# Optimization experiments

Hardware: AMD Instinct MI355X
Metric: run time of the kernel (lower is better)

Reference implementation:

```python
import jax, jax.numpy as jnp
import numpy as np

N = 50000   # nodes
E = 600000  # edges (before self-loops)
D = 128     # input_dim
H = 128     # hidden_dim
NEG_SLOPE = 0.2  # GATConv default


def setup_inputs() -> dict:
    key = jax.random.key(0)
    ks = jax.random.split(key, 16)
    inp = {
        "x": jax.random.normal(ks[0], (N, D), jnp.float32),
        "edge_index": jax.random.randint(ks[1], (2, E), 0, N, dtype=jnp.int64),
        "edge_attr": jax.random.normal(ks[2], (E, 1), jnp.float32),
    }
    # GATConv params per layer: lin W [H,in] (no bias), att_src/att_dst [H],
    # lin_edge We [H,1] (no bias), att_edge [H], final bias b [H]
    def mk(k, shape, fan_in):
        return jax.random.normal(k, shape, jnp.float32) / np.sqrt(fan_in)
    ins = [D, H]
    ki = 3
    for i in range(2):
        cin = ins[i]
        inp[f"W{i}"] = mk(ks[ki], (H, cin), cin); ki += 1
        inp[f"att_src{i}"] = mk(ks[ki], (H,), H); ki += 1
        inp[f"att_dst{i}"] = mk(ks[ki], (H,), H); ki += 1
        inp[f"We{i}"] = mk(ks[ki], (H, 1), 1); ki += 1
        inp[f"att_e{i}"] = mk(ks[ki], (H,), H); ki += 1
        inp[f"b{i}"] = jnp.zeros((H,), jnp.float32)
    return inp


def _gat_forward(x, edge_index, edge_attr, params):
    # add self loops; self-loop edge_attr = mean of edge_attr (fill_value='mean')
    src = jnp.concatenate([edge_index[0], jnp.arange(N, dtype=edge_index.dtype)])
    dst = jnp.concatenate([edge_index[1], jnp.arange(N, dtype=edge_index.dtype)])
    ea = jnp.concatenate(
        [edge_attr, jnp.broadcast_to(edge_attr.mean(0, keepdims=True), (N, 1))], 0
    )  # [E+N, 1]

    def gat_layer(h, W, b, a_s, a_d, We, a_e):
        hp = h @ W.T                                   # [N, H]
        e_lin = ea @ We.T                              # [E+N, H]
        alpha = (hp @ a_s)[src] + (hp @ a_d)[dst] + e_lin @ a_e  # [E+N]
        alpha = jax.nn.leaky_relu(alpha, NEG_SLOPE)
        # segment softmax over destination nodes
        m = jax.ops.segment_max(alpha, dst, num_segments=N)
        m = jnp.where(jnp.isfinite(m), m, 0.0)
        w = jnp.exp(alpha - m[dst])
        denom = jax.ops.segment_sum(w, dst, num_segments=N)
        w = w / (denom[dst] + 1e-16)
        out = jax.ops.segment_sum(hp[src] * w[:, None], dst, num_segments=N)
        return out + b

    layer_outs = [x]
    h = x
    for i in range(2):
        h = jax.nn.relu(
            gat_layer(h, params[f"W{i}"], params[f"b{i}"], params[f"att_src{i}"],
                      params[f"att_dst{i}"], params[f"We{i}"], params[f"att_e{i}"])
        )
        layer_outs.append(h)
    return jnp.concatenate(layer_outs, axis=-1)  # JK 'cat': [N, D + 2H]


def reference(x, edge_index, edge_attr,
              W0, att_src0, att_dst0, We0, att_e0, b0,
              W1, att_src1, att_dst1, We1, att_e1, b1):
    params = {
        "W0": W0, "att_src0": att_src0, "att_dst0": att_dst0, "We0": We0,
        "att_e0": att_e0, "b0": b0,
        "W1": W1, "att_src1": att_src1, "att_dst1": att_dst1, "We1": We1,
        "att_e1": att_e1, "b1": b1,
    }
    return _gat_forward(x, edge_index, edge_attr, params)
```

## Files before the change

### kernel.cpp

```cpp
#include <hip/hip_runtime.h>
#include <hip/hip_fp16.h>
#include <math.h>

#define N_NODES 50000
#define N_EDGES 600000
#define TOT (N_EDGES + N_NODES)
#define HD 128
#define OUTW 384
#define NEG_SLOPE 0.2f


typedef _Float16 h2_t __attribute__((ext_vector_type(2)));

static __device__ __forceinline__ float fdot2f(h2_t a, h2_t b, float c){
#if __has_builtin(__builtin_amdgcn_fdot2)
  return __builtin_amdgcn_fdot2(a, b, c, false);
#else
  return fmaf((float)a[0], (float)b[0], fmaf((float)a[1], (float)b[1], c));
#endif
}

static __device__ __forceinline__ int load_edge(const void* ei, int is64, long long off){
  return is64 ? (int)((const long long*)ei)[off] : ((const int*)ei)[off];
}


__global__ __launch_bounds__(256) void prep_kernel(const void* ei, int* flag,
                                                   const float* __restrict__ We0, const float* __restrict__ ae0,
                                                   const float* __restrict__ We1, const float* __restrict__ ae1,
                                                   float* scal, const float* __restrict__ eattr){
  int t = threadIdx.x;
  if (blockIdx.x == 0){
    __shared__ float buf[128];
    __shared__ int okbuf;
    if (t == 0) okbuf = 1;
    __syncthreads();
    if (t < 64){
      long long v = ((const long long*)ei)[t];
      if (v < 0 || v >= N_NODES) atomicAnd(&okbuf, 0);
    }
    if (t < 128) buf[t] = We0[t] * ae0[t];
    __syncthreads();
    for (int off = 64; off > 0; off >>= 1){ if (t < off) buf[t] += buf[t + off]; __syncthreads(); }
    if (t == 0) scal[1] = buf[0];
    __syncthreads();
    if (t < 128) buf[t] = We1[t] * ae1[t];
    __syncthreads();
    for (int off = 64; off > 0; off >>= 1){ if (t < off) buf[t] += buf[t + off]; __syncthreads(); }
    if (t == 0){ scal[2] = buf[0]; *flag = okbuf; }
  }
  int tid = blockIdx.x * 256 + t;
  float s = 0.f;
  for (int i = tid; i < N_EDGES; i += 256 * 256) s += eattr[i];
  for (int off = 32; off > 0; off >>= 1) s += __shfl_down(s, off, 64);
  __shared__ float ws[4];
  int lane = t & 63, w = t >> 6;
  if (lane == 0) ws[w] = s;
  __syncthreads();
  if (t == 0) atomicAdd(&scal[0], ws[0] + ws[1] + ws[2] + ws[3]);
}

#define XBLK 6250
#define WBLK 64
#define DBLK 2540
__global__ __launch_bounds__(256) void conv_kernel(const float* __restrict__ x,
                                                   __half* __restrict__ x16,
                                                   float* __restrict__ out,
                                                   const float* __restrict__ W0, const float* __restrict__ W1,
                                                   __half2* __restrict__ Wt0, __half2* __restrict__ Wt1,
                                                   const void* ei, const int* flag, int* deg,
                                                   int* __restrict__ src32, int* __restrict__ dst32){
  int b = blockIdx.x;
  if (b < XBLK){
    int idx = b * 256 + threadIdx.x;
    int n = idx >> 5, c4 = idx & 31;
    float4 v = ((const float4*)x)[idx];
    *(float4*)&out[(size_t)n * OUTW + c4 * 4] = v;
    float2 pk;
    ((__half2*)&pk)[0] = __floats2half2_rn(v.x, v.y);
    ((__half2*)&pk)[1] = __floats2half2_rn(v.z, v.w);
    *(float2*)&x16[(size_t)idx * 4] = pk;
  } else if (b < XBLK + WBLK){
    int e = (b - XBLK) * 256 + threadIdx.x;
    const float* W = (e < 8192) ? W0 : W1;
    __half2* Wt = (e < 8192) ? Wt0 : Wt1;
    int i = e & 8191;
    int n = i & 127, k2 = i >> 7;
    float a = W[n * HD + 2 * k2];
    float c = W[n * HD + 2 * k2 + 1];
    Wt[k2 * 128 + n] = __floats2half2_rn(a, c);
  } else {
    int e = (b - XBLK - WBLK) * 256 + threadIdx.x;
    if (e >= TOT) return;
    int is64 = *flag;
    int d;
    if (e < N_EDGES){
      int s = load_edge(ei, is64, e);
      d = load_edge(ei, is64, (long long)N_EDGES + e);
      src32[e] = s;
      dst32[e] = d;
    } else {
      d = e - N_EDGES;
    }
    atomicAdd(&deg[d], 1);
  }
}

__global__ __launch_bounds__(256) void scan_chunk_kernel(const int* __restrict__ deg,
                                                         int* __restrict__ rowstart,
                                                         int* __restrict__ chunksums){
  __shared__ int sums[256];
  int t = threadIdx.x;
  int base = blockIdx.x * 1024 + t * 4;
  int v[4];
  #pragma unroll
  for (int i = 0; i < 4; i++) v[i] = (base + i < N_NODES) ? deg[base + i] : 0;
  int tsum = v[0] + v[1] + v[2] + v[3];
  sums[t] = tsum;
  __syncthreads();
  for (int off = 1; off < 256; off <<= 1){
    int add = (t >= off) ? sums[t - off] : 0;
    __syncthreads();
    sums[t] += add;
    __syncthreads();
  }
  int run = sums[t] - tsum;
  #pragma unroll
  for (int i = 0; i < 4; i++){
    if (base + i < N_NODES) rowstart[base + i] = run;
    run += v[i];
  }
  if (t == 255) chunksums[blockIdx.x] = sums[255];
}

__global__ __launch_bounds__(256) void add_off_kernel(int* rowstart, int* rowcur,
                                                      const int* __restrict__ chunksums){
  __shared__ int soff;
  int t = threadIdx.x;
  if (t < 64){
    int v = (t < blockIdx.x) ? chunksums[t] : 0;
    for (int o = 32; o > 0; o >>= 1) v += __shfl_down(v, o, 64);
    if (t == 0) soff = v;
  }
  __syncthreads();
  int off = soff;
  int base = blockIdx.x * 1024 + t * 4;
  #pragma unroll
  for (int i = 0; i < 4; i++){
    if (base + i < N_NODES){
      int v = rowstart[base + i] + off;
      rowstart[base + i] = v;
      rowcur[base + i] = v;
    }
  }
}

__global__ __launch_bounds__(256) void fill_kernel(const int* __restrict__ src32,
                                                   const int* __restrict__ dst32,
                                                   int* rowcur, int2* __restrict__ csr){
  int e = blockIdx.x * 256 + threadIdx.x;
  if (e >= TOT) return;
  int s, d;
  if (e < N_EDGES){
    s = src32[e];
    d = dst32[e];
  } else {
    s = d = e - N_EDGES;
  }
  int pos = atomicAdd(&rowcur[d], 1);
  csr[pos] = make_int2(s, e);
}


#define BM 128

__global__ __launch_bounds__(256, 2) void gemm_kernel(const __half* __restrict__ hin,
                                                      const __half2* __restrict__ Wt,
                                                      __half* __restrict__ hp_h,
                                                      const float* __restrict__ as_,
                                                      const float* __restrict__ ad_,
                                                      float* __restrict__ ssrc,
                                                      float* __restrict__ sdst){
  __shared__ __half2 As2[64 * 128];
  __shared__ __half2 Wh2[64 * 128];
  int t  = threadIdx.x;
  int tx = t & 15;
  int ty = t >> 4;
  int rb = blockIdx.x * BM;

  {
    const float4* src = (const float4*)Wt;
    float4* dst = (float4*)Wh2;
    #pragma unroll
    for (int p = 0; p < 8; p++) dst[t + p * 256] = src[t + p * 256];
  }
  #pragma unroll
  for (int p = 0; p < 8; p++){
    int idx = t + p * 256;
    int row = idx >> 4, c8 = idx & 15;
    int gr = rb + row; if (gr >= N_NODES) gr = N_NODES - 1;
    float4 v = *(const float4*)&hin[(size_t)gr * HD + c8 * 8];
    __half2* hv = (__half2*)&v;
    #pragma unroll
    for (int q = 0; q < 4; q++) As2[(4 * c8 + q) * 128 + row] = hv[q];
  }
  __syncthreads();

  float acc[8][8];
  #pragma unroll
  for (int i = 0; i < 8; i++)
    #pragma unroll
    for (int j = 0; j < 8; j++) acc[i][j] = 0.f;

  #pragma unroll 4
  for (int k2 = 0; k2 < 64; k2++){
    float4 ar0 = *(const float4*)&As2[k2 * 128 + ty * 8];
    float4 ar1 = *(const float4*)&As2[k2 * 128 + ty * 8 + 4];
    float4 wr0 = *(const float4*)&Wh2[k2 * 128 + tx * 4];
    float4 wr1 = *(const float4*)&Wh2[k2 * 128 + 64 + tx * 4];
    const h2_t* av0 = (const h2_t*)&ar0;
    const h2_t* av1 = (const h2_t*)&ar1;
    const h2_t* wv0 = (const h2_t*)&wr0;
    const h2_t* wv1 = (const h2_t*)&wr1;
    #pragma unroll
    for (int i = 0; i < 8; i++){
      h2_t ai = (i < 4) ? av0[i] : av1[i - 4];
      #pragma unroll
      for (int j = 0; j < 4; j++){
        acc[i][j]     = fdot2f(ai, wv0[j], acc[i][j]);
        acc[i][j + 4] = fdot2f(ai, wv1[j], acc[i][j + 4]);
      }
    }
  }

  #pragma unroll
  for (int i = 0; i < 8; i++){
    int r = rb + ty * 8 + i;
    if (r < N_NODES){
      float2 s0, s1;
      ((__half2*)&s0)[0] = __floats2half2_rn(acc[i][0], acc[i][1]);
      ((__half2*)&s0)[1] = __floats2half2_rn(acc[i][2], acc[i][3]);
      ((__half2*)&s1)[0] = __floats2half2_rn(acc[i][4], acc[i][5]);
      ((__half2*)&s1)[1] = __floats2half2_rn(acc[i][6], acc[i][7]);
      *(float2*)&hp_h[(size_t)r * HD + tx * 4]      = s0;
      *(float2*)&hp_h[(size_t)r * HD + 64 + tx * 4] = s1;
    }
  }

  float as_v[8], ad_v[8];
  #pragma unroll
  for (int j = 0; j < 4; j++){
    as_v[j]     = as_[tx * 4 + j];      ad_v[j]     = ad_[tx * 4 + j];
    as_v[j + 4] = as_[64 + tx * 4 + j]; ad_v[j + 4] = ad_[64 + tx * 4 + j];
  }
  #pragma unroll
  for (int i = 0; i < 8; i++){
    float ps = 0.f, pd = 0.f;
    #pragma unroll
    for (int j = 0; j < 8; j++){
      ps = fmaf(acc[i][j], as_v[j], ps);
      pd = fmaf(acc[i][j], ad_v[j], pd);
    }
    #pragma unroll
    for (int off = 8; off > 0; off >>= 1){
      ps += __shfl_down(ps, off, 16);
      pd += __shfl_down(pd, off, 16);
    }
    int r = rb + ty * 8 + i;
    if (tx == 0 && r < N_NODES){ ssrc[r] = ps; sdst[r] = pd; }
  }
}

__global__ __launch_bounds__(256) void agg_kernel(const int* __restrict__ rowstart,
                                                  const int2* __restrict__ csr,
                                                  const float* __restrict__ eattr,
                                                  const float* __restrict__ ssrc,
                                                  const float* __restrict__ sdst,
                                                  const float* __restrict__ scal, int which,
                                                  const __half* __restrict__ hp_h,
                                                  const float* __restrict__ bias,
                                                  __half* __restrict__ hnext,
                                                  float* __restrict__ out, int outoff){
  int sub  = threadIdx.x >> 4;
  int lane = threadIdx.x & 15;
  int n = blockIdx.x * 16 + sub;
  if (n >= N_NODES) return;
  int s0 = rowstart[n];
  int s1 = (n + 1 < N_NODES) ? rowstart[n + 1] : TOT;
  float sd = sdst[n];
  float ce = scal[1 + which];
  float mean_ea = scal[0] * (1.0f / (float)N_EDGES);
  const float4* hb = (const float4*)hp_h;

  float a0 = 0.f, a1 = 0.f, a2 = 0.f, a3 = 0.f;
  float a4 = 0.f, a5 = 0.f, a6 = 0.f, a7 = 0.f;
  float sum = 0.f;

#define EW(se) ({ float eav = ((se).y < N_EDGES) ? eattr[(se).y] : mean_ea;       \
    float al = ssrc[(se).x] + sd + eav * ce;                                      \
    al = (al >= 0.f) ? al : NEG_SLOPE * al;                                       \
    expf(al); })

#define ACC8(r, p) { const __half2* hh = (const __half2*)&(r); float2 f;         \
    f = __half22float2(hh[0]); a0 = fmaf(p, f.x, a0); a1 = fmaf(p, f.y, a1);     \
    f = __half22float2(hh[1]); a2 = fmaf(p, f.x, a2); a3 = fmaf(p, f.y, a3);     \
    f = __half22float2(hh[2]); a4 = fmaf(p, f.x, a4); a5 = fmaf(p, f.y, a5);     \
    f = __half22float2(hh[3]); a6 = fmaf(p, f.x, a6); a7 = fmaf(p, f.y, a7); }

  int i = s0;
  for (; i + 4 <= s1; i += 4){
    int2 se0 = csr[i],     se1 = csr[i + 1];
    int2 se2 = csr[i + 2], se3 = csr[i + 3];
    float4 r0 = hb[(size_t)se0.x * 16 + lane];
    float4 r1 = hb[(size_t)se1.x * 16 + lane];
    float4 r2 = hb[(size_t)se2.x * 16 + lane];
    float4 r3 = hb[(size_t)se3.x * 16 + lane];
    float p0 = EW(se0), p1 = EW(se1), p2 = EW(se2), p3 = EW(se3);
    sum += p0 + p1 + p2 + p3;
    ACC8(r0, p0); ACC8(r1, p1); ACC8(r2, p2); ACC8(r3, p3);
  }
  for (; i < s1; i++){
    int2 se = csr[i];
    float4 r = hb[(size_t)se.x * 16 + lane];
    float p = EW(se);
    sum += p;
    ACC8(r, p);
  }
#undef ACC8
#undef EW

  float inv = 1.0f / (sum + 1e-16f);
  float4 bA = *(const float4*)&bias[lane * 8];
  float4 bB = *(const float4*)&bias[lane * 8 + 4];
  float v0 = fmaf(a0, inv, bA.x); v0 = v0 > 0.f ? v0 : 0.f;
  float v1 = fmaf(a1, inv, bA.y); v1 = v1 > 0.f ? v1 : 0.f;
  float v2 = fmaf(a2, inv, bA.z); v2 = v2 > 0.f ? v2 : 0.f;
  float v3 = fmaf(a3, inv, bA.w); v3 = v3 > 0.f ? v3 : 0.f;
  float v4 = fmaf(a4, inv, bB.x); v4 = v4 > 0.f ? v4 : 0.f;
  float v5 = fmaf(a5, inv, bB.y); v5 = v5 > 0.f ? v5 : 0.f;
  float v6 = fmaf(a6, inv, bB.z); v6 = v6 > 0.f ? v6 : 0.f;
  float v7 = fmaf(a7, inv, bB.w); v7 = v7 > 0.f ? v7 : 0.f;
  if (hnext){
    float4 pk;
    __half2* p2h = (__half2*)&pk;
    p2h[0] = __floats2half2_rn(v0, v1);
    p2h[1] = __floats2half2_rn(v2, v3);
    p2h[2] = __floats2half2_rn(v4, v5);
    p2h[3] = __floats2half2_rn(v6, v7);
    *(float4*)&hnext[(size_t)n * HD + lane * 8] = pk;
  }
  *(float4*)&out[(size_t)n * OUTW + outoff + lane * 8]     = make_float4(v0, v1, v2, v3);
  *(float4*)&out[(size_t)n * OUTW + outoff + lane * 8 + 4] = make_float4(v4, v5, v6, v7);
}


extern "C" void kernel_launch(void* const* d_in, const int* in_sizes, int n_in,
                              void* d_out, int out_size, void* d_ws, size_t ws_size,
                              hipStream_t stream){
  (void)in_sizes; (void)n_in; (void)out_size; (void)ws_size;
  const float* x    = (const float*)d_in[0];
  const void*  ei   = d_in[1];
  const float* eatt = (const float*)d_in[2];
  const float* W0   = (const float*)d_in[3];
  const float* as0  = (const float*)d_in[4];
  const float* ad0  = (const float*)d_in[5];
  const float* We0  = (const float*)d_in[6];
  const float* ae0  = (const float*)d_in[7];
  const float* b0   = (const float*)d_in[8];
  const float* W1   = (const float*)d_in[9];
  const float* as1  = (const float*)d_in[10];
  const float* ad1  = (const float*)d_in[11];
  const float* We1  = (const float*)d_in[12];
  const float* ae1  = (const float*)d_in[13];
  const float* b1   = (const float*)d_in[14];
  float* out = (float*)d_out;

  char* ws = (char*)d_ws;
  size_t off = 0;
  auto alloc = [&](size_t bytes) -> void* {
    void* p = ws + off;
    off += (bytes + 255) & ~(size_t)255;
    return p;
  };
  __half*   hp_h     = (__half*)  alloc((size_t)N_NODES * HD * 2);
  __half*   h1       = (__half*)  alloc((size_t)N_NODES * HD * 2);
  __half*   x16      = (__half*)  alloc((size_t)N_NODES * HD * 2);
  float*    ssrc     = (float*)   alloc((size_t)N_NODES * 4);
  float*    sdst     = (float*)   alloc((size_t)N_NODES * 4);
  int*      deg      = (int*)     alloc((size_t)N_NODES * 4);
  float*    scal     = (float*)   alloc(64 * 4);
  int*      rowstart = (int*)     alloc((size_t)N_NODES * 4);
  int*      rowcur   = (int*)     alloc((size_t)N_NODES * 4);
  int*      src32    = (int*)     alloc((size_t)N_EDGES * 4);
  int*      dst32    = (int*)     alloc((size_t)N_EDGES * 4);
  int2*     csr      = (int2*)    alloc((size_t)TOT * 8);
  __half2*  Wt0      = (__half2*) alloc((size_t)8192 * 4);
  __half2*  Wt1      = (__half2*) alloc((size_t)8192 * 4);
  int*      chunksums= (int*)     alloc(64 * 4);
  int*      flag     = (int*)     alloc(64);

  hipMemsetAsync(deg, 0, 200192 + 256, stream);

  const int nchunks = (N_NODES + 1023) / 1024;
  const int FB = (TOT + 255) / 256;

  prep_kernel<<<256, 256, 0, stream>>>(ei, flag, We0, ae0, We1, ae1, scal, eatt);
  conv_kernel<<<XBLK + WBLK + DBLK, 256, 0, stream>>>(x, x16, out, W0, W1, Wt0, Wt1,
                                                      ei, flag, deg, src32, dst32);
  scan_chunk_kernel<<<nchunks, 256, 0, stream>>>(deg, rowstart, chunksums);
  add_off_kernel<<<nchunks, 256, 0, stream>>>(rowstart, rowcur, chunksums);
  fill_kernel<<<FB, 256, 0, stream>>>(src32, dst32, rowcur, csr);

  const int GB = (N_NODES + BM - 1) / BM;
  const int NB16 = (N_NODES + 15) / 16;

  gemm_kernel<<<GB, 256, 0, stream>>>(x16, Wt0, hp_h, as0, ad0, ssrc, sdst);
  agg_kernel<<<NB16, 256, 0, stream>>>(rowstart, csr, eatt, ssrc, sdst, scal, 0, hp_h, b0, h1, out, 128);

  gemm_kernel<<<GB, 256, 0, stream>>>(h1, Wt1, hp_h, as1, ad1, ssrc, sdst);
  agg_kernel<<<NB16, 256, 0, stream>>>(rowstart, csr, eatt, ssrc, sdst, scal, 1, hp_h, b1, nullptr, out, 256);
}
```

Before: 324.6 us.

## Fuse all GAT stages into one persistent kernel with grid-wide barriers

Replaces the nine separate launches (prep, convert, scan, offset, fill, two GEMMs, two aggregations) with a single persistent kernel of 512 blocks. Stages are separated by a software grid barrier built on atomic counters. The aim is to remove per-launch overhead and idle gaps between small kernels. The aggregation inner loop is also unrolled to 8 edges to give more gathers in flight. In exchange, each stage is capped at 512 resident blocks, and the barrier assumes all blocks are co-resident; it has a spin timeout that could silently break ordering.

```diff
diff --git a/kernel.cpp b/kernel.cpp
--- a/kernel.cpp
+++ b/kernel.cpp
@@ -9,6 +9,14 @@
 #define OUTW 384
 #define NEG_SLOPE 0.2f
 
+#define GRID 512
+#define NTHR 256
+#define GSZ (GRID * NTHR)
+#define NCHUNK 49
+#define BM 128
+#define GB 391
+#define AGB 3125
+
 
 typedef _Float16 h2_t __attribute__((ext_vector_type(2)));
 
@@ -24,97 +32,111 @@
   return is64 ? (int)((const long long*)ei)[off] : ((const int*)ei)[off];
 }
 
-
-__global__ __launch_bounds__(256) void prep_kernel(const void* ei, int* flag,
-                                                   const float* __restrict__ We0, const float* __restrict__ ae0,
-                                                   const float* __restrict__ We1, const float* __restrict__ ae1,
-                                                   float* scal, const float* __restrict__ eattr){
-  int t = threadIdx.x;
-  if (blockIdx.x == 0){
-    __shared__ float buf[128];
-    __shared__ int okbuf;
-    if (t == 0) okbuf = 1;
-    __syncthreads();
-    if (t < 64){
-      long long v = ((const long long*)ei)[t];
-      if (v < 0 || v >= N_NODES) atomicAnd(&okbuf, 0);
-    }
-    if (t < 128) buf[t] = We0[t] * ae0[t];
-    __syncthreads();
-    for (int off = 64; off > 0; off >>= 1){ if (t < off) buf[t] += buf[t + off]; __syncthreads(); }
-    if (t == 0) scal[1] = buf[0];
-    __syncthreads();
-    if (t < 128) buf[t] = We1[t] * ae1[t];
-    __syncthreads();
-    for (int off = 64; off > 0; off >>= 1){ if (t < off) buf[t] += buf[t + off]; __syncthreads(); }
-    if (t == 0){ scal[2] = buf[0]; *flag = okbuf; }
-  }
-  int tid = blockIdx.x * 256 + t;
-  float s = 0.f;
-  for (int i = tid; i < N_EDGES; i += 256 * 256) s += eattr[i];
-  for (int off = 32; off > 0; off >>= 1) s += __shfl_down(s, off, 64);
-  __shared__ float ws[4];
-  int lane = t & 63, w = t >> 6;
-  if (lane == 0) ws[w] = s;
-  __syncthreads();
-  if (t == 0) atomicAdd(&scal[0], ws[0] + ws[1] + ws[2] + ws[3]);
-}
-
-#define XBLK 6250
-#define WBLK 64
-#define DBLK 2540
-__global__ __launch_bounds__(256) void conv_kernel(const float* __restrict__ x,
-                                                   __half* __restrict__ x16,
-                                                   float* __restrict__ out,
-                                                   const float* __restrict__ W0, const float* __restrict__ W1,
-                                                   __half2* __restrict__ Wt0, __half2* __restrict__ Wt1,
-                                                   const void* ei, const int* flag, int* deg,
-                                                   int* __restrict__ src32, int* __restrict__ dst32){
-  int b = blockIdx.x;
-  if (b < XBLK){
-    int idx = b * 256 + threadIdx.x;
+struct MegaArgs {
+  const float* x; const void* ei; const float* eattr;
+  const float* W0; const float* as0; const float* ad0; const float* b0;
+  const float* W1; const float* as1; const float* ad1; const float* b1;
+  const float* We0; const float* ae0; const float* We1; const float* ae1;
+  __half* x16; __half* hp_h; __half* h1;
+  float* ssrc; float* sdst;
+  int* deg; float* scal;
+  int* rowstart; int* rowcur;
+  int* src32; int* dst32; int2* csr;
+  __half2* Wt0; __half2* Wt1; int* chunksums;
+  int* barcnt; int* bargen;
+  float* out;
+};
+
+__device__ __forceinline__ void gbar(int* cnt, int* gen){
+  __syncthreads();
+  if (threadIdx.x == 0){
+    __threadfence();
+    int g = __hip_atomic_load(gen, __ATOMIC_RELAXED, __HIP_MEMORY_SCOPE_AGENT);
+    int arrived = __hip_atomic_fetch_add(cnt, 1, __ATOMIC_ACQ_REL, __HIP_MEMORY_SCOPE_AGENT);
+    if (arrived == GRID - 1){
+      __hip_atomic_store(cnt, 0, __ATOMIC_RELAXED, __HIP_MEMORY_SCOPE_AGENT);
+      __hip_atomic_fetch_add(gen, 1, __ATOMIC_RELEASE, __HIP_MEMORY_SCOPE_AGENT);
+    } else {
+      long long spins = 0;
+      while (__hip_atomic_load(gen, __ATOMIC_RELAXED, __HIP_MEMORY_SCOPE_AGENT) == g){
+        __builtin_amdgcn_s_sleep(2);
+        if (++spins > (1LL << 22)) break;
+      }
+    }
+    __threadfence();
+  }
+  __syncthreads();
+}
+
+
+__device__ __forceinline__ void dev_phase0(int bid, int t, const MegaArgs& a, int* s_is64){
+  if (t < 64){
+    long long v = ((const long long*)a.ei)[t];
+    unsigned long long bad = __ballot(v < 0 || v >= N_NODES);
+    if (t == 0) *s_is64 = (bad == 0ull) ? 1 : 0;
+  }
+  __syncthreads();
+  int is64 = *s_is64;
+  int gtid = bid * NTHR + t;
+
+  for (int idx = gtid; idx < N_NODES * HD / 4; idx += GSZ){
     int n = idx >> 5, c4 = idx & 31;
-    float4 v = ((const float4*)x)[idx];
-    *(float4*)&out[(size_t)n * OUTW + c4 * 4] = v;
+    float4 v = ((const float4*)a.x)[idx];
+    *(float4*)&a.out[(size_t)n * OUTW + c4 * 4] = v;
     float2 pk;
     ((__half2*)&pk)[0] = __floats2half2_rn(v.x, v.y);
     ((__half2*)&pk)[1] = __floats2half2_rn(v.z, v.w);
-    *(float2*)&x16[(size_t)idx * 4] = pk;
-  } else if (b < XBLK + WBLK){
-    int e = (b - XBLK) * 256 + threadIdx.x;
-    const float* W = (e < 8192) ? W0 : W1;
-    __half2* Wt = (e < 8192) ? Wt0 : Wt1;
+    *(float2*)&a.x16[(size_t)idx * 4] = pk;
+  }
+  for (int e = gtid; e < 16384; e += GSZ){
+    const float* W = (e < 8192) ? a.W0 : a.W1;
+    __half2* Wt = (e < 8192) ? a.Wt0 : a.Wt1;
     int i = e & 8191;
     int n = i & 127, k2 = i >> 7;
-    float a = W[n * HD + 2 * k2];
-    float c = W[n * HD + 2 * k2 + 1];
-    Wt[k2 * 128 + n] = __floats2half2_rn(a, c);
-  } else {
-    int e = (b - XBLK - WBLK) * 256 + threadIdx.x;
-    if (e >= TOT) return;
-    int is64 = *flag;
+    float va = W[n * HD + 2 * k2];
+    float vb = W[n * HD + 2 * k2 + 1];
+    Wt[k2 * 128 + n] = __floats2half2_rn(va, vb);
+  }
+  for (int e = gtid; e < TOT; e += GSZ){
     int d;
     if (e < N_EDGES){
-      int s = load_edge(ei, is64, e);
-      d = load_edge(ei, is64, (long long)N_EDGES + e);
-      src32[e] = s;
-      dst32[e] = d;
+      int s = load_edge(a.ei, is64, e);
+      d = load_edge(a.ei, is64, (long long)N_EDGES + e);
+      a.src32[e] = s;
+      a.dst32[e] = d;
     } else {
       d = e - N_EDGES;
     }
-    atomicAdd(&deg[d], 1);
-  }
-}
-
-__global__ __launch_bounds__(256) void scan_chunk_kernel(const int* __restrict__ deg,
-                                                         int* __restrict__ rowstart,
-                                                         int* __restrict__ chunksums){
-  __shared__ int sums[256];
-  int t = threadIdx.x;
-  int base = blockIdx.x * 1024 + t * 4;
+    atomicAdd(&a.deg[d], 1);
+  }
+  {
+    float s = 0.f;
+    for (int i = gtid; i < N_EDGES; i += GSZ) s += a.eattr[i];
+    #pragma unroll
+    for (int o = 32; o > 0; o >>= 1) s += __shfl_down(s, o, 64);
+    if ((t & 63) == 0) atomicAdd(&a.scal[0], s);
+  }
+  if (bid == 0){
+    int w = t >> 6, lane = t & 63;
+    if (w == 1){
+      float s = a.We0[lane] * a.ae0[lane] + a.We0[lane + 64] * a.ae0[lane + 64];
+      #pragma unroll
+      for (int o = 32; o > 0; o >>= 1) s += __shfl_down(s, o, 64);
+      if (lane == 0) a.scal[1] = s;
+    } else if (w == 2){
+      float s = a.We1[lane] * a.ae1[lane] + a.We1[lane + 64] * a.ae1[lane + 64];
+      #pragma unroll
+      for (int o = 32; o > 0; o >>= 1) s += __shfl_down(s, o, 64);
+      if (lane == 0) a.scal[2] = s;
+    }
+  }
+}
+
+__device__ __forceinline__ void dev_scanC(int bid, int t, int* sums, const MegaArgs& a){
+  int base = bid * 1024 + t * 4;
   int v[4];
   #pragma unroll
-  for (int i = 0; i < 4; i++) v[i] = (base + i < N_NODES) ? deg[base + i] : 0;
+  for (int i = 0; i < 4; i++) v[i] = (base + i < N_NODES) ? a.deg[base + i] : 0;
   int tsum = v[0] + v[1] + v[2] + v[3];
   sums[t] = tsum;
   __syncthreads();
@@ -127,66 +149,55 @@
   int run = sums[t] - tsum;
   #pragma unroll
   for (int i = 0; i < 4; i++){
-    if (base + i < N_NODES) rowstart[base + i] = run;
+    if (base + i < N_NODES) a.rowstart[base + i] = run;
     run += v[i];
   }
-  if (t == 255) chunksums[blockIdx.x] = sums[255];
-}
-
-__global__ __launch_bounds__(256) void add_off_kernel(int* rowstart, int* rowcur,
-                                                      const int* __restrict__ chunksums){
-  __shared__ int soff;
-  int t = threadIdx.x;
-  if (t < 64){
-    int v = (t < blockIdx.x) ? chunksums[t] : 0;
-    for (int o = 32; o > 0; o >>= 1) v += __shfl_down(v, o, 64);
-    if (t == 0) soff = v;
-  }
-  __syncthreads();
-  int off = soff;
-  int base = blockIdx.x * 1024 + t * 4;
+  if (t == 255) a.chunksums[bid] = sums[255];
+}
+
+__device__ __forceinline__ void dev_offD(int bid, int t, const MegaArgs& a){
+  int lane = t & 63;
+  int v = (lane < bid) ? a.chunksums[lane] : 0;
+  #pragma unroll
+  for (int o = 32; o > 0; o >>= 1) v += __shfl_down(v, o, 64);
+  int off = __shfl(v, 0, 64);
+  int base = bid * 1024 + t * 4;
   #pragma unroll
   for (int i = 0; i < 4; i++){
     if (base + i < N_NODES){
-      int v = rowstart[base + i] + off;
-      rowstart[base + i] = v;
-      rowcur[base + i] = v;
-    }
-  }
-}
-
-__global__ __launch_bounds__(256) void fill_kernel(const int* __restrict__ src32,
-                                                   const int* __restrict__ dst32,
-                                                   int* rowcur, int2* __restrict__ csr){
-  int e = blockIdx.x * 256 + threadIdx.x;
-  if (e >= TOT) return;
-  int s, d;
-  if (e < N_EDGES){
-    s = src32[e];
-    d = dst32[e];
-  } else {
-    s = d = e - N_EDGES;
-  }
-  int pos = atomicAdd(&rowcur[d], 1);
-  csr[pos] = make_int2(s, e);
-}
-
-
-#define BM 128
-
-__global__ __launch_bounds__(256, 2) void gemm_kernel(const __half* __restrict__ hin,
-                                                      const __half2* __restrict__ Wt,
-                                                      __half* __restrict__ hp_h,
-                                                      const float* __restrict__ as_,
-                                                      const float* __restrict__ ad_,
-                                                      float* __restrict__ ssrc,
-                                                      float* __restrict__ sdst){
-  __shared__ __half2 As2[64 * 128];
-  __shared__ __half2 Wh2[64 * 128];
-  int t  = threadIdx.x;
+      int r = a.rowstart[base + i] + off;
+      a.rowstart[base + i] = r;
+      a.rowcur[base + i] = r;
+    }
+  }
+}
+
+__device__ __forceinline__ void dev_fillE(int bid, int t, const MegaArgs& a){
+  int gtid = bid * NTHR + t;
+  for (int e = gtid; e < TOT; e += GSZ){
+    int s, d;
+    if (e < N_EDGES){
+      s = a.src32[e];
+      d = a.dst32[e];
+    } else {
+      s = d = e - N_EDGES;
+    }
+    int pos = atomicAdd(&a.rowcur[d], 1);
+    a.csr[pos] = make_int2(s, e);
+  }
+}
+
+__device__ __forceinline__ void dev_gemm_tile(int tb, int t, __half2* As2, __half2* Wh2,
+                                              const __half* __restrict__ hin,
+                                              const __half2* __restrict__ Wt,
+                                              __half* __restrict__ hp_h,
+                                              const float* __restrict__ as_,
+                                              const float* __restrict__ ad_,
+                                              float* __restrict__ ssrc,
+                                              float* __restrict__ sdst){
   int tx = t & 15;
   int ty = t >> 4;
-  int rb = blockIdx.x * BM;
+  int rb = tb * BM;
 
   {
     const float4* src = (const float4*)Wt;
@@ -269,32 +280,37 @@
     int r = rb + ty * 8 + i;
     if (tx == 0 && r < N_NODES){ ssrc[r] = ps; sdst[r] = pd; }
   }
-}
-
-__global__ __launch_bounds__(256) void agg_kernel(const int* __restrict__ rowstart,
-                                                  const int2* __restrict__ csr,
-                                                  const float* __restrict__ eattr,
-                                                  const float* __restrict__ ssrc,
-                                                  const float* __restrict__ sdst,
-                                                  const float* __restrict__ scal, int which,
-                                                  const __half* __restrict__ hp_h,
-                                                  const float* __restrict__ bias,
-                                                  __half* __restrict__ hnext,
-                                                  float* __restrict__ out, int outoff){
-  int sub  = threadIdx.x >> 4;
-  int lane = threadIdx.x & 15;
-  int n = blockIdx.x * 16 + sub;
-  if (n >= N_NODES) return;
-  int s0 = rowstart[n];
-  int s1 = (n + 1 < N_NODES) ? rowstart[n + 1] : TOT;
-  float sd = sdst[n];
+  __syncthreads();
+}
+
+__device__ __forceinline__ void dev_agg(int bid, int t,
+                                        const int* __restrict__ rowstart,
+                                        const int2* __restrict__ csr,
+                                        const float* __restrict__ eattr,
+                                        const float* __restrict__ ssrc,
+                                        const float* __restrict__ sdst,
+                                        const float* __restrict__ scal, int which,
+                                        const __half* __restrict__ hp_h,
+                                        const float* __restrict__ bias,
+                                        __half* __restrict__ hnext,
+                                        float* __restrict__ out, int outoff){
+  int sub  = t >> 4;
+  int lane = t & 15;
   float ce = scal[1 + which];
   float mean_ea = scal[0] * (1.0f / (float)N_EDGES);
+  float4 bA = *(const float4*)&bias[lane * 8];
+  float4 bB = *(const float4*)&bias[lane * 8 + 4];
   const float4* hb = (const float4*)hp_h;
 
-  float a0 = 0.f, a1 = 0.f, a2 = 0.f, a3 = 0.f;
-  float a4 = 0.f, a5 = 0.f, a6 = 0.f, a7 = 0.f;
-  float sum = 0.f;
+  for (int nb = bid; nb < AGB; nb += GRID){
+    int n = nb * 16 + sub;
+    int s0 = rowstart[n];
+    int s1 = (n + 1 < N_NODES) ? rowstart[n + 1] : TOT;
+    float sd = sdst[n];
+
+    float a0 = 0.f, a1 = 0.f, a2 = 0.f, a3 = 0.f;
+    float a4 = 0.f, a5 = 0.f, a6 = 0.f, a7 = 0.f;
+    float sum = 0.f;
 
 #define EW(se) ({ float eav = ((se).y < N_EDGES) ? eattr[(se).y] : mean_ea;       \
     float al = ssrc[(se).x] + sd + eav * ce;                                      \
@@ -307,50 +323,81 @@
     f = __half22float2(hh[2]); a4 = fmaf(p, f.x, a4); a5 = fmaf(p, f.y, a5);     \
     f = __half22float2(hh[3]); a6 = fmaf(p, f.x, a6); a7 = fmaf(p, f.y, a7); }
 
-  int i = s0;
-  for (; i + 4 <= s1; i += 4){
-    int2 se0 = csr[i],     se1 = csr[i + 1];
-    int2 se2 = csr[i + 2], se3 = csr[i + 3];
-    float4 r0 = hb[(size_t)se0.x * 16 + lane];
-    float4 r1 = hb[(size_t)se1.x * 16 + lane];
-    float4 r2 = hb[(size_t)se2.x * 16 + lane];
-    float4 r3 = hb[(size_t)se3.x * 16 + lane];
-    float p0 = EW(se0), p1 = EW(se1), p2 = EW(se2), p3 = EW(se3);
-    sum += p0 + p1 + p2 + p3;
-    ACC8(r0, p0); ACC8(r1, p1); ACC8(r2, p2); ACC8(r3, p3);
-  }
-  for (; i < s1; i++){
-    int2 se = csr[i];
-    float4 r = hb[(size_t)se.x * 16 + lane];
-    float p = EW(se);
-    sum += p;
-    ACC8(r, p);
-  }
+    int i = s0;
+    for (; i + 8 <= s1; i += 8){
+      int2 se[8]; float4 r[8];
+      #pragma unroll
+      for (int u = 0; u < 8; u++) se[u] = csr[i + u];
+      #pragma unroll
+      for (int u = 0; u < 8; u++) r[u] = hb[(size_t)se[u].x * 16 + lane];
+      #pragma unroll
+      for (int u = 0; u < 8; u++){
+        float p = EW(se[u]);
+        sum += p;
+        ACC8(r[u], p);
+      }
+    }
+    for (; i < s1; i++){
+      int2 se = csr[i];
+      float4 r = hb[(size_t)se.x * 16 + lane];
+      float p = EW(se);
+      sum += p;
+      ACC8(r, p);
+    }
 #undef ACC8
 #undef EW
 
-  float inv = 1.0f / (sum + 1e-16f);
-  float4 bA = *(const float4*)&bias[lane * 8];
-  float4 bB = *(const float4*)&bias[lane * 8 + 4];
-  float v0 = fmaf(a0, inv, bA.x); v0 = v0 > 0.f ? v0 : 0.f;
-  float v1 = fmaf(a1, inv, bA.y); v1 = v1 > 0.f ? v1 : 0.f;
-  float v2 = fmaf(a2, inv, bA.z); v2 = v2 > 0.f ? v2 : 0.f;
-  float v3 = fmaf(a3, inv, bA.w); v3 = v3 > 0.f ? v3 : 0.f;
-  float v4 = fmaf(a4, inv, bB.x); v4 = v4 > 0.f ? v4 : 0.f;
-  float v5 = fmaf(a5, inv, bB.y); v5 = v5 > 0.f ? v5 : 0.f;
-  float v6 = fmaf(a6, inv, bB.z); v6 = v6 > 0.f ? v6 : 0.f;
-  float v7 = fmaf(a7, inv, bB.w); v7 = v7 > 0.f ? v7 : 0.f;
-  if (hnext){
-    float4 pk;
-    __half2* p2h = (__half2*)&pk;
-    p2h[0] = __floats2half2_rn(v0, v1);
-    p2h[1] = __floats2half2_rn(v2, v3);
-    p2h[2] = __floats2half2_rn(v4, v5);
-    p2h[3] = __floats2half2_rn(v6, v7);
-    *(float4*)&hnext[(size_t)n * HD + lane * 8] = pk;
-  }
-  *(float4*)&out[(size_t)n * OUTW + outoff + lane * 8]     = make_float4(v0, v1, v2, v3);
-  *(float4*)&out[(size_t)n * OUTW + outoff + lane * 8 + 4] = make_float4(v4, v5, v6, v7);
+    float inv = 1.0f / (sum + 1e-16f);
+    float v0 = fmaf(a0, inv, bA.x); v0 = v0 > 0.f ? v0 : 0.f;
+    float v1 = fmaf(a1, inv, bA.y); v1 = v1 > 0.f ? v1 : 0.f;
+    float v2 = fmaf(a2, inv, bA.z); v2 = v2 > 0.f ? v2 : 0.f;
+    float v3 = fmaf(a3, inv, bA.w); v3 = v3 > 0.f ? v3 : 0.f;
+    float v4 = fmaf(a4, inv, bB.x); v4 = v4 > 0.f ? v4 : 0.f;
+    float v5 = fmaf(a5, inv, bB.y); v5 = v5 > 0.f ? v5 : 0.f;
+    float v6 = fmaf(a6, inv, bB.z); v6 = v6 > 0.f ? v6 : 0.f;
+    float v7 = fmaf(a7, inv, bB.w); v7 = v7 > 0.f ? v7 : 0.f;
+    if (hnext){
+      float4 pk;
+      __half2* p2h = (__half2*)&pk;
+      p2h[0] = __floats2half2_rn(v0, v1);
+      p2h[1] = __floats2half2_rn(v2, v3);
+      p2h[2] = __floats2half2_rn(v4, v5);
+      p2h[3] = __floats2half2_rn(v6, v7);
+      *(float4*)&hnext[(size_t)n * HD + lane * 8] = pk;
+    }
+    *(float4*)&out[(size_t)n * OUTW + outoff + lane * 8]     = make_float4(v0, v1, v2, v3);
+    *(float4*)&out[(size_t)n * OUTW + outoff + lane * 8 + 4] = make_float4(v4, v5, v6, v7);
+  }
+}
+
+
+__global__ __launch_bounds__(256, 2) void mega_kernel(MegaArgs a){
+  __shared__ __align__(16) char smraw[65536];
+  __half2* smA = (__half2*)smraw;
+  __half2* smW = (__half2*)(smraw + 32768);
+  int* isums = (int*)smraw;
+  int* s_is64 = (int*)(smraw + 65280);
+
+  int bid = blockIdx.x, t = threadIdx.x;
+
+  dev_phase0(bid, t, a, s_is64);
+  gbar(a.barcnt, a.bargen);
+  if (bid < NCHUNK) dev_scanC(bid, t, isums, a);
+  gbar(a.barcnt, a.bargen);
+  if (bid < NCHUNK) dev_offD(bid, t, a);
+  gbar(a.barcnt, a.bargen);
+  dev_fillE(bid, t, a);
+  for (int tb = bid; tb < GB; tb += GRID)
+    dev_gemm_tile(tb, t, smA, smW, a.x16, a.Wt0, a.hp_h, a.as0, a.ad0, a.ssrc, a.sdst);
+  gbar(a.barcnt, a.bargen);
+  dev_agg(bid, t, a.rowstart, a.csr, a.eattr, a.ssrc, a.sdst,
+          a.scal, 0, a.hp_h, a.b0, a.h1, a.out, 128);
+  gbar(a.barcnt, a.bargen);
+  for (int tb = bid; tb < GB; tb += GRID)
+    dev_gemm_tile(tb, t, smA, smW, a.h1, a.Wt1, a.hp_h, a.as1, a.ad1, a.ssrc, a.sdst);
+  gbar(a.barcnt, a.bargen);
+  dev_agg(bid, t, a.rowstart, a.csr, a.eattr, a.ssrc, a.sdst,
+          a.scal, 1, a.hp_h, a.b1, nullptr, a.out, 256);
 }
 
 
@@ -358,22 +405,6 @@
                               void* d_out, int out_size, void* d_ws, size_t ws_size,
                               hipStream_t stream){
   (void)in_sizes; (void)n_in; (void)out_size; (void)ws_size;
-  const float* x    = (const float*)d_in[0];
-  const void*  ei   = d_in[1];
-  const float* eatt = (const float*)d_in[2];
-  const float* W0   = (const float*)d_in[3];
-  const float* as0  = (const float*)d_in[4];
-  const float* ad0  = (const float*)d_in[5];
-  const float* We0  = (const float*)d_in[6];
-  const float* ae0  = (const float*)d_in[7];
-  const float* b0   = (const float*)d_in[8];
-  const float* W1   = (const float*)d_in[9];
-  const float* as1  = (const float*)d_in[10];
-  const float* ad1  = (const float*)d_in[11];
-  const float* We1  = (const float*)d_in[12];
-  const float* ae1  = (const float*)d_in[13];
-  const float* b1   = (const float*)d_in[14];
-  float* out = (float*)d_out;
 
   char* ws = (char*)d_ws;
   size_t off = 0;
@@ -382,41 +413,47 @@
     off += (bytes + 255) & ~(size_t)255;
     return p;
   };
-  __half*   hp_h     = (__half*)  alloc((size_t)N_NODES * HD * 2);
-  __half*   h1       = (__half*)  alloc((size_t)N_NODES * HD * 2);
-  __half*   x16      = (__half*)  alloc((size_t)N_NODES * HD * 2);
-  float*    ssrc     = (float*)   alloc((size_t)N_NODES * 4);
-  float*    sdst     = (float*)   alloc((size_t)N_NODES * 4);
-  int*      deg      = (int*)     alloc((size_t)N_NODES * 4);
-  float*    scal     = (float*)   alloc(64 * 4);
-  int*      rowstart = (int*)     alloc((size_t)N_NODES * 4);
-  int*      rowcur   = (int*)     alloc((size_t)N_NODES * 4);
-  int*      src32    = (int*)     alloc((size_t)N_EDGES * 4);
-  int*      dst32    = (int*)     alloc((size_t)N_EDGES * 4);
-  int2*     csr      = (int2*)    alloc((size_t)TOT * 8);
-  __half2*  Wt0      = (__half2*) alloc((size_t)8192 * 4);
-  __half2*  Wt1      = (__half2*) alloc((size_t)8192 * 4);
-  int*      chunksums= (int*)     alloc(64 * 4);
-  int*      flag     = (int*)     alloc(64);
-
-  hipMemsetAsync(deg, 0, 200192 + 256, stream);
-
-  const int nchunks = (N_NODES + 1023) / 1024;
-  const int FB = (TOT + 255) / 256;
-
-  prep_kernel<<<256, 256, 0, stream>>>(ei, flag, We0, ae0, We1, ae1, scal, eatt);
-  conv_kernel<<<XBLK + WBLK + DBLK, 256, 0, stream>>>(x, x16, out, W0, W1, Wt0, Wt1,
-                                                      ei, flag, deg, src32, dst32);
-  scan_chunk_kernel<<<nchunks, 256, 0, stream>>>(deg, rowstart, chunksums);
-  add_off_kernel<<<nchunks, 256, 0, stream>>>(rowstart, rowcur, chunksums);
-  fill_kernel<<<FB, 256, 0, stream>>>(src32, dst32, rowcur, csr);
-
-  const int GB = (N_NODES + BM - 1) / BM;
-  const int NB16 = (N_NODES + 15) / 16;
-
-  gemm_kernel<<<GB, 256, 0, stream>>>(x16, Wt0, hp_h, as0, ad0, ssrc, sdst);
-  agg_kernel<<<NB16, 256, 0, stream>>>(rowstart, csr, eatt, ssrc, sdst, scal, 0, hp_h, b0, h1, out, 128);
-
-  gemm_kernel<<<GB, 256, 0, stream>>>(h1, Wt1, hp_h, as1, ad1, ssrc, sdst);
-  agg_kernel<<<NB16, 256, 0, stream>>>(rowstart, csr, eatt, ssrc, sdst, scal, 1, hp_h, b1, nullptr, out, 256);
-}
+
+  MegaArgs a;
+  a.x    = (const float*)d_in[0];
+  a.ei   = d_in[1];
+  a.eattr= (const float*)d_in[2];
+  a.W0   = (const float*)d_in[3];
+  a.as0  = (const float*)d_in[4];
+  a.ad0  = (const float*)d_in[5];
+  a.We0  = (const float*)d_in[6];
+  a.ae0  = (const float*)d_in[7];
+  a.b0   = (const float*)d_in[8];
+  a.W1   = (const float*)d_in[9];
+  a.as1  = (const float*)d_in[10];
+  a.ad1  = (const float*)d_in[11];
+  a.We1  = (const float*)d_in[12];
+  a.ae1  = (const float*)d_in[13];
+  a.b1   = (const float*)d_in[14];
+  a.out  = (float*)d_out;
+
+  a.hp_h     = (__half*)  alloc((size_t)N_NODES * HD * 2);
+  a.h1       = (__half*)  alloc((size_t)N_NODES * HD * 2);
+  a.x16      = (__half*)  alloc((size_t)N_NODES * HD * 2);
+  a.ssrc     = (float*)   alloc((size_t)N_NODES * 4);
+  a.sdst     = (float*)   alloc((size_t)N_NODES * 4);
+  a.deg      = (int*)     alloc((size_t)N_NODES * 4);
+  a.scal     = (float*)   alloc(256);
+  {
+    int* bar = (int*)alloc(256);
+    a.barcnt = bar;
+    a.bargen = bar + 32;
+  }
+  a.rowstart = (int*)     alloc((size_t)N_NODES * 4);
+  a.rowcur   = (int*)     alloc((size_t)N_NODES * 4);
+  a.src32    = (int*)     alloc((size_t)N_EDGES * 4);
+  a.dst32    = (int*)     alloc((size_t)N_EDGES * 4);
+  a.csr      = (int2*)    alloc((size_t)TOT * 8);
+  a.Wt0      = (__half2*) alloc((size_t)8192 * 4);
+  a.Wt1      = (__half2*) alloc((size_t)8192 * 4);
+  a.chunksums= (int*)     alloc(64 * 4);
+
+  hipMemsetAsync(a.deg, 0, 200192 + 256 + 256, stream);
+
+  mega_kernel<<<GRID, NTHR, 0, stream>>>(a);
+}
```

After: 541.4 us. 1.67x slower.

## Fuse prep into conversion kernel and overlap CSR fill with first GEMM

Applied to the files above, without the earlier changes.

Folds the edge-attribute mean, the attention-edge scalars and the int64 detection into extra block ranges of the conversion kernel, removing the separate prep launch. The CSR fill now runs as extra blocks inside the first GEMM launch, since the layer-0 GEMM does not depend on the CSR. The GEMM moves to 512-thread blocks with 4 rows per thread, and the aggregation loop is unrolled to 8 gathers in flight. This cuts launches and serialization points, at the cost of higher register pressure and heterogeneous blocks sharing one launch.

```diff
diff --git a/kernel.cpp b/kernel.cpp
--- a/kernel.cpp
+++ b/kernel.cpp
@@ -9,6 +9,17 @@
 #define OUTW 384
 #define NEG_SLOPE 0.2f
 
+#define BM 128
+#define GB 391
+#define AGB 3125
+#define NCHUNK 49
+#define FILLB 256
+
+#define XBLK 6250
+#define WBLK 64
+#define DBLK 2540
+#define SBLK 64
+
 
 typedef _Float16 h2_t __attribute__((ext_vector_type(2)));
 
@@ -24,55 +35,20 @@
   return is64 ? (int)((const long long*)ei)[off] : ((const int*)ei)[off];
 }
 
-
-__global__ __launch_bounds__(256) void prep_kernel(const void* ei, int* flag,
-                                                   const float* __restrict__ We0, const float* __restrict__ ae0,
-                                                   const float* __restrict__ We1, const float* __restrict__ ae1,
-                                                   float* scal, const float* __restrict__ eattr){
-  int t = threadIdx.x;
-  if (blockIdx.x == 0){
-    __shared__ float buf[128];
-    __shared__ int okbuf;
-    if (t == 0) okbuf = 1;
-    __syncthreads();
-    if (t < 64){
-      long long v = ((const long long*)ei)[t];
-      if (v < 0 || v >= N_NODES) atomicAnd(&okbuf, 0);
-    }
-    if (t < 128) buf[t] = We0[t] * ae0[t];
-    __syncthreads();
-    for (int off = 64; off > 0; off >>= 1){ if (t < off) buf[t] += buf[t + off]; __syncthreads(); }
-    if (t == 0) scal[1] = buf[0];
-    __syncthreads();
-    if (t < 128) buf[t] = We1[t] * ae1[t];
-    __syncthreads();
-    for (int off = 64; off > 0; off >>= 1){ if (t < off) buf[t] += buf[t + off]; __syncthreads(); }
-    if (t == 0){ scal[2] = buf[0]; *flag = okbuf; }
-  }
-  int tid = blockIdx.x * 256 + t;
-  float s = 0.f;
-  for (int i = tid; i < N_EDGES; i += 256 * 256) s += eattr[i];
-  for (int off = 32; off > 0; off >>= 1) s += __shfl_down(s, off, 64);
-  __shared__ float ws[4];
-  int lane = t & 63, w = t >> 6;
-  if (lane == 0) ws[w] = s;
-  __syncthreads();
-  if (t == 0) atomicAdd(&scal[0], ws[0] + ws[1] + ws[2] + ws[3]);
-}
-
-#define XBLK 6250
-#define WBLK 64
-#define DBLK 2540
 __global__ __launch_bounds__(256) void conv_kernel(const float* __restrict__ x,
                                                    __half* __restrict__ x16,
                                                    float* __restrict__ out,
                                                    const float* __restrict__ W0, const float* __restrict__ W1,
                                                    __half2* __restrict__ Wt0, __half2* __restrict__ Wt1,
-                                                   const void* ei, const int* flag, int* deg,
-                                                   int* __restrict__ src32, int* __restrict__ dst32){
+                                                   const void* ei, int* deg,
+                                                   int* __restrict__ src32, int* __restrict__ dst32,
+                                                   const float* __restrict__ eattr, float* scal,
+                                                   const float* __restrict__ We0, const float* __restrict__ ae0,
+                                                   const float* __restrict__ We1, const float* __restrict__ ae1){
   int b = blockIdx.x;
+  int t = threadIdx.x;
   if (b < XBLK){
-    int idx = b * 256 + threadIdx.x;
+    int idx = b * 256 + t;
     int n = idx >> 5, c4 = idx & 31;
     float4 v = ((const float4*)x)[idx];
     *(float4*)&out[(size_t)n * OUTW + c4 * 4] = v;
@@ -81,7 +57,7 @@
     ((__half2*)&pk)[1] = __floats2half2_rn(v.z, v.w);
     *(float2*)&x16[(size_t)idx * 4] = pk;
   } else if (b < XBLK + WBLK){
-    int e = (b - XBLK) * 256 + threadIdx.x;
+    int e = (b - XBLK) * 256 + t;
     const float* W = (e < 8192) ? W0 : W1;
     __half2* Wt = (e < 8192) ? Wt0 : Wt1;
     int i = e & 8191;
@@ -89,22 +65,51 @@
     float a = W[n * HD + 2 * k2];
     float c = W[n * HD + 2 * k2 + 1];
     Wt[k2 * 128 + n] = __floats2half2_rn(a, c);
+  } else if (b < XBLK + WBLK + DBLK){
+    __shared__ int s_is64;
+    if (t < 64){
+      long long v = ((const long long*)ei)[t];
+      unsigned long long bad = __ballot(v < 0 || v >= N_NODES);
+      if (t == 0) s_is64 = (bad == 0ull) ? 1 : 0;
+    }
+    __syncthreads();
+    int is64 = s_is64;
+    int e = (b - XBLK - WBLK) * 256 + t;
+    if (e < TOT){
+      int d;
+      if (e < N_EDGES){
+        int s = load_edge(ei, is64, e);
+        d = load_edge(ei, is64, (long long)N_EDGES + e);
+        src32[e] = s;
+        dst32[e] = d;
+      } else {
+        d = e - N_EDGES;
+      }
+      atomicAdd(&deg[d], 1);
+    }
+  } else if (b < XBLK + WBLK + DBLK + SBLK){
+    int gtid = (b - XBLK - WBLK - DBLK) * 256 + t;
+    float s = 0.f;
+    for (int i = gtid; i < N_EDGES; i += SBLK * 256) s += eattr[i];
+    #pragma unroll
+    for (int o = 32; o > 0; o >>= 1) s += __shfl_down(s, o, 64);
+    if ((t & 63) == 0) atomicAdd(&scal[0], s);
   } else {
-    int e = (b - XBLK - WBLK) * 256 + threadIdx.x;
-    if (e >= TOT) return;
-    int is64 = *flag;
-    int d;
-    if (e < N_EDGES){
-      int s = load_edge(ei, is64, e);
-      d = load_edge(ei, is64, (long long)N_EDGES + e);
-      src32[e] = s;
-      dst32[e] = d;
-    } else {
-      d = e - N_EDGES;
-    }
-    atomicAdd(&deg[d], 1);
-  }
-}
+    int w = t >> 6, lane = t & 63;
+    if (w == 1){
+      float s = We0[lane] * ae0[lane] + We0[lane + 64] * ae0[lane + 64];
+      #pragma unroll
+      for (int o = 32; o > 0; o >>= 1) s += __shfl_down(s, o, 64);
+      if (lane == 0) scal[1] = s;
+    } else if (w == 2){
+      float s = We1[lane] * ae1[lane] + We1[lane + 64] * ae1[lane + 64];
+      #pragma unroll
+      for (int o = 32; o > 0; o >>= 1) s += __shfl_down(s, o, 64);
+      if (lane == 0) scal[2] = s;
+    }
+  }
+}
+
 
 __global__ __launch_bounds__(256) void scan_chunk_kernel(const int* __restrict__ deg,
                                                          int* __restrict__ rowstart,
@@ -155,48 +160,27 @@
   }
 }
 
-__global__ __launch_bounds__(256) void fill_kernel(const int* __restrict__ src32,
-                                                   const int* __restrict__ dst32,
-                                                   int* rowcur, int2* __restrict__ csr){
-  int e = blockIdx.x * 256 + threadIdx.x;
-  if (e >= TOT) return;
-  int s, d;
-  if (e < N_EDGES){
-    s = src32[e];
-    d = dst32[e];
-  } else {
-    s = d = e - N_EDGES;
-  }
-  int pos = atomicAdd(&rowcur[d], 1);
-  csr[pos] = make_int2(s, e);
-}
-
-
-#define BM 128
-
-__global__ __launch_bounds__(256, 2) void gemm_kernel(const __half* __restrict__ hin,
-                                                      const __half2* __restrict__ Wt,
-                                                      __half* __restrict__ hp_h,
-                                                      const float* __restrict__ as_,
-                                                      const float* __restrict__ ad_,
-                                                      float* __restrict__ ssrc,
-                                                      float* __restrict__ sdst){
-  __shared__ __half2 As2[64 * 128];
-  __shared__ __half2 Wh2[64 * 128];
-  int t  = threadIdx.x;
+__device__ __forceinline__ void gemm_tile512(int tb, int t, __half2* As2, __half2* Wh2,
+                                             const __half* __restrict__ hin,
+                                             const __half2* __restrict__ Wt,
+                                             __half* __restrict__ hp_h,
+                                             const float* __restrict__ as_,
+                                             const float* __restrict__ ad_,
+                                             float* __restrict__ ssrc,
+                                             float* __restrict__ sdst){
   int tx = t & 15;
   int ty = t >> 4;
-  int rb = blockIdx.x * BM;
+  int rb = tb * BM;
 
   {
     const float4* src = (const float4*)Wt;
     float4* dst = (float4*)Wh2;
     #pragma unroll
-    for (int p = 0; p < 8; p++) dst[t + p * 256] = src[t + p * 256];
-  }
-  #pragma unroll
-  for (int p = 0; p < 8; p++){
-    int idx = t + p * 256;
+    for (int p = 0; p < 4; p++) dst[t + p * 512] = src[t + p * 512];
+  }
+  #pragma unroll
+  for (int p = 0; p < 4; p++){
+    int idx = t + p * 512;
     int row = idx >> 4, c8 = idx & 15;
     int gr = rb + row; if (gr >= N_NODES) gr = N_NODES - 1;
     float4 v = *(const float4*)&hin[(size_t)gr * HD + c8 * 8];
@@ -206,25 +190,23 @@
   }
   __syncthreads();
 
-  float acc[8][8];
-  #pragma unroll
-  for (int i = 0; i < 8; i++)
+  float acc[4][8];
+  #pragma unroll
+  for (int i = 0; i < 4; i++)
     #pragma unroll
     for (int j = 0; j < 8; j++) acc[i][j] = 0.f;
 
   #pragma unroll 4
   for (int k2 = 0; k2 < 64; k2++){
-    float4 ar0 = *(const float4*)&As2[k2 * 128 + ty * 8];
-    float4 ar1 = *(const float4*)&As2[k2 * 128 + ty * 8 + 4];
+    float4 ar0 = *(const float4*)&As2[k2 * 128 + ty * 4];
     float4 wr0 = *(const float4*)&Wh2[k2 * 128 + tx * 4];
     float4 wr1 = *(const float4*)&Wh2[k2 * 128 + 64 + tx * 4];
-    const h2_t* av0 = (const h2_t*)&ar0;
-    const h2_t* av1 = (const h2_t*)&ar1;
+    const h2_t* av = (const h2_t*)&ar0;
     const h2_t* wv0 = (const h2_t*)&wr0;
     const h2_t* wv1 = (const h2_t*)&wr1;
     #pragma unroll
-    for (int i = 0; i < 8; i++){
-      h2_t ai = (i < 4) ? av0[i] : av1[i - 4];
+    for (int i = 0; i < 4; i++){
+      h2_t ai = av[i];
       #pragma unroll
       for (int j = 0; j < 4; j++){
         acc[i][j]     = fdot2f(ai, wv0[j], acc[i][j]);
@@ -234,8 +216,8 @@
   }
 
   #pragma unroll
-  for (int i = 0; i < 8; i++){
-    int r = rb + ty * 8 + i;
+  for (int i = 0; i < 4; i++){
+    int r = rb + ty * 4 + i;
     if (r < N_NODES){
       float2 s0, s1;
       ((__half2*)&s0)[0] = __floats2half2_rn(acc[i][0], acc[i][1]);
@@ -254,7 +236,7 @@
     as_v[j + 4] = as_[64 + tx * 4 + j]; ad_v[j + 4] = ad_[64 + tx * 4 + j];
   }
   #pragma unroll
-  for (int i = 0; i < 8; i++){
+  for (int i = 0; i < 4; i++){
     float ps = 0.f, pd = 0.f;
     #pragma unroll
     for (int j = 0; j < 8; j++){
@@ -266,9 +248,52 @@
       ps += __shfl_down(ps, off, 16);
       pd += __shfl_down(pd, off, 16);
     }
-    int r = rb + ty * 8 + i;
+    int r = rb + ty * 4 + i;
     if (tx == 0 && r < N_NODES){ ssrc[r] = ps; sdst[r] = pd; }
   }
+}
+
+__global__ __launch_bounds__(512, 4) void fillgemm_kernel(const __half* __restrict__ hin,
+                                                          const __half2* __restrict__ Wt,
+                                                          __half* __restrict__ hp_h,
+                                                          const float* __restrict__ as_,
+                                                          const float* __restrict__ ad_,
+                                                          float* __restrict__ ssrc,
+                                                          float* __restrict__ sdst,
+                                                          const int* __restrict__ src32,
+                                                          const int* __restrict__ dst32,
+                                                          int* rowcur, int2* __restrict__ csr){
+  __shared__ __align__(16) __half2 As2[64 * 128];
+  __shared__ __align__(16) __half2 Wh2[64 * 128];
+  int b = blockIdx.x;
+  if (b < GB){
+    gemm_tile512(b, threadIdx.x, As2, Wh2, hin, Wt, hp_h, as_, ad_, ssrc, sdst);
+  } else {
+    int gtid = (b - GB) * 512 + threadIdx.x;
+    for (int e = gtid; e < TOT; e += FILLB * 512){
+      int s, d;
+      if (e < N_EDGES){
+        s = src32[e];
+        d = dst32[e];
+      } else {
+        s = d = e - N_EDGES;
+      }
+      int pos = atomicAdd(&rowcur[d], 1);
+      csr[pos] = make_int2(s, e);
+    }
+  }
+}
+
+__global__ __launch_bounds__(512, 4) void gemm_kernel(const __half* __restrict__ hin,
+                                                      const __half2* __restrict__ Wt,
+                                                      __half* __restrict__ hp_h,
+                                                      const float* __restrict__ as_,
+                                                      const float* __restrict__ ad_,
+                                                      float* __restrict__ ssrc,
+                                                      float* __restrict__ sdst){
+  __shared__ __align__(16) __half2 As2[64 * 128];
+  __shared__ __align__(16) __half2 Wh2[64 * 128];
+  gemm_tile512(blockIdx.x, threadIdx.x, As2, Wh2, hin, Wt, hp_h, as_, ad_, ssrc, sdst);
 }
 
 __global__ __launch_bounds__(256) void agg_kernel(const int* __restrict__ rowstart,
@@ -284,12 +309,13 @@
   int sub  = threadIdx.x >> 4;
   int lane = threadIdx.x & 15;
   int n = blockIdx.x * 16 + sub;
-  if (n >= N_NODES) return;
   int s0 = rowstart[n];
   int s1 = (n + 1 < N_NODES) ? rowstart[n + 1] : TOT;
   float sd = sdst[n];
   float ce = scal[1 + which];
   float mean_ea = scal[0] * (1.0f / (float)N_EDGES);
+  float4 bA = *(const float4*)&bias[lane * 8];
+  float4 bB = *(const float4*)&bias[lane * 8 + 4];
   const float4* hb = (const float4*)hp_h;
 
   float a0 = 0.f, a1 = 0.f, a2 = 0.f, a3 = 0.f;
@@ -308,16 +334,18 @@
     f = __half22float2(hh[3]); a6 = fmaf(p, f.x, a6); a7 = fmaf(p, f.y, a7); }
 
   int i = s0;
-  for (; i + 4 <= s1; i += 4){
-    int2 se0 = csr[i],     se1 = csr[i + 1];
-    int2 se2 = csr[i + 2], se3 = csr[i + 3];
-    float4 r0 = hb[(size_t)se0.x * 16 + lane];
-    float4 r1 = hb[(size_t)se1.x * 16 + lane];
-    float4 r2 = hb[(size_t)se2.x * 16 + lane];
-    float4 r3 = hb[(size_t)se3.x * 16 + lane];
-    float p0 = EW(se0), p1 = EW(se1), p2 = EW(se2), p3 = EW(se3);
-    sum += p0 + p1 + p2 + p3;
-    ACC8(r0, p0); ACC8(r1, p1); ACC8(r2, p2); ACC8(r3, p3);
+  for (; i + 8 <= s1; i += 8){
+    int2 se[8]; float4 r[8];
+    #pragma unroll
+    for (int u = 0; u < 8; u++) se[u] = csr[i + u];
+    #pragma unroll
+    for (int u = 0; u < 8; u++) r[u] = hb[(size_t)se[u].x * 16 + lane];
+    #pragma unroll
+    for (int u = 0; u < 8; u++){
+      float p = EW(se[u]);
+      sum += p;
+      ACC8(r[u], p);
+    }
   }
   for (; i < s1; i++){
     int2 se = csr[i];
@@ -330,8 +358,6 @@
 #undef EW
 
   float inv = 1.0f / (sum + 1e-16f);
-  float4 bA = *(const float4*)&bias[lane * 8];
-  float4 bB = *(const float4*)&bias[lane * 8 + 4];
   float v0 = fmaf(a0, inv, bA.x); v0 = v0 > 0.f ? v0 : 0.f;
   float v1 = fmaf(a1, inv, bA.y); v1 = v1 > 0.f ? v1 : 0.f;
   float v2 = fmaf(a2, inv, bA.z); v2 = v2 > 0.f ? v2 : 0.f;
@@ -388,7 +414,7 @@
   float*    ssrc     = (float*)   alloc((size_t)N_NODES * 4);
   float*    sdst     = (float*)   alloc((size_t)N_NODES * 4);
   int*      deg      = (int*)     alloc((size_t)N_NODES * 4);
-  float*    scal     = (float*)   alloc(64 * 4);
+  float*    scal     = (float*)   alloc(256);
   int*      rowstart = (int*)     alloc((size_t)N_NODES * 4);
   int*      rowcur   = (int*)     alloc((size_t)N_NODES * 4);
   int*      src32    = (int*)     alloc((size_t)N_EDGES * 4);
@@ -397,26 +423,21 @@
   __half2*  Wt0      = (__half2*) alloc((size_t)8192 * 4);
   __half2*  Wt1      = (__half2*) alloc((size_t)8192 * 4);
   int*      chunksums= (int*)     alloc(64 * 4);
-  int*      flag     = (int*)     alloc(64);
 
   hipMemsetAsync(deg, 0, 200192 + 256, stream);
 
-  const int nchunks = (N_NODES + 1023) / 1024;
-  const int FB = (TOT + 255) / 256;
-
-  prep_kernel<<<256, 256, 0, stream>>>(ei, flag, We0, ae0, We1, ae1, scal, eatt);
-  conv_kernel<<<XBLK + WBLK + DBLK, 256, 0, stream>>>(x, x16, out, W0, W1, Wt0, Wt1,
-                                                      ei, flag, deg, src32, dst32);
-  scan_chunk_kernel<<<nchunks, 256, 0, stream>>>(deg, rowstart, chunksums);
-  add_off_kernel<<<nchunks, 256, 0, stream>>>(rowstart, rowcur, chunksums);
-  fill_kernel<<<FB, 256, 0, stream>>>(src32, dst32, rowcur, csr);
-
-  const int GB = (N_NODES + BM - 1) / BM;
-  const int NB16 = (N_NODES + 15) / 16;
-
-  gemm_kernel<<<GB, 256, 0, stream>>>(x16, Wt0, hp_h, as0, ad0, ssrc, sdst);
-  agg_kernel<<<NB16, 256, 0, stream>>>(rowstart, csr, eatt, ssrc, sdst, scal, 0, hp_h, b0, h1, out, 128);
-
-  gemm_kernel<<<GB, 256, 0, stream>>>(h1, Wt1, hp_h, as1, ad1, ssrc, sdst);
-  agg_kernel<<<NB16, 256, 0, stream>>>(rowstart, csr, eatt, ssrc, sdst, scal, 1, hp_h, b1, nullptr, out, 256);
-}
+  conv_kernel<<<XBLK + WBLK + DBLK + SBLK + 1, 256, 0, stream>>>(
+      x, x16, out, W0, W1, Wt0, Wt1, ei, deg, src32, dst32, eatt, scal,
+      We0, ae0, We1, ae1);
+  scan_chunk_kernel<<<NCHUNK, 256, 0, stream>>>(deg, rowstart, chunksums);
+  add_off_kernel<<<NCHUNK, 256, 0, stream>>>(rowstart, rowcur, chunksums);
+
+  fillgemm_kernel<<<GB + FILLB, 512, 0, stream>>>(x16, Wt0, hp_h, as0, ad0, ssrc, sdst,
+                                                  src32, dst32, rowcur, csr);
+  agg_kernel<<<AGB, 256, 0, stream>>>(rowstart, csr, eatt, ssrc, sdst, scal, 0,
+                                      hp_h, b0, h1, out, 128);
+
+  gemm_kernel<<<GB, 512, 0, stream>>>(h1, Wt1, hp_h, as1, ad1, ssrc, sdst);
+  agg_kernel<<<AGB, 256, 0, stream>>>(rowstart, csr, eatt, ssrc, sdst, scal, 1,
+                                      hp_h, b1, nullptr, out, 256);
+}
```

Measured after the change: 311.2 us. 1.04x faster.
